# Performance work log

Hardware: AMD Instinct MI355X
Metric: run time of the kernel (lower is better)

The kernel has to match this reference:

```python
import jax, jax.numpy as jnp
import numpy as np

N, E, D, G = 50000, 600000, 128, 512  # nodes, edges, embed_dim, graphs-per-batch
LN_EPS = 1e-5


def setup_inputs() -> dict:
    key = jax.random.key(0)
    ks = jax.random.split(key, 8)
    node_hidden = jax.random.normal(ks[0], (N, D), dtype=jnp.float32)
    edge_hidden = jax.random.normal(ks[1], (E, D), dtype=jnp.float32)
    # GINEConv MLP params: Linear(D, 2D) -> ReLU -> Linear(2D, D)
    W1 = jax.random.normal(ks[2], (D, 2 * D), dtype=jnp.float32) * (1.0 / np.sqrt(D))
    b1 = jnp.zeros((2 * D,), dtype=jnp.float32)
    W2 = jax.random.normal(ks[3], (2 * D, D), dtype=jnp.float32) * (1.0 / np.sqrt(2 * D))
    b2 = jnp.zeros((D,), dtype=jnp.float32)
    ln_gamma = jnp.ones((D,), dtype=jnp.float32)
    ln_beta = jnp.zeros((D,), dtype=jnp.float32)
    edge_index = jax.random.randint(ks[4], (2, E), 0, N, dtype=jnp.int32)
    node_id = jnp.sort(jax.random.randint(ks[5], (N,), 0, G, dtype=jnp.int32))
    edge_id = jnp.sort(jax.random.randint(ks[6], (E,), 0, G, dtype=jnp.int32))
    return {
        "node_hidden": node_hidden, "edge_hidden": edge_hidden,
        "W1": W1, "b1": b1, "W2": W2, "b2": b2,
        "ln_gamma": ln_gamma, "ln_beta": ln_beta,
        "edge_index": edge_index, "node_id": node_id, "edge_id": edge_id,
    }


def reference(node_hidden, edge_hidden, W1, b1, W2, b2, ln_gamma, ln_beta,
              edge_index, node_id, edge_id):
    n = node_hidden.shape[0]
    src, dst = edge_index[0], edge_index[1]
    # --- GINEConv: msg = relu(x_src + e), scatter-add at dst, (1+eps)*x + agg, MLP ---
    msg = jax.nn.relu(node_hidden[src] + edge_hidden)          # [E, D]
    agg = jax.ops.segment_sum(msg, dst, num_segments=n)        # [N, D]
    h = node_hidden + agg                                      # eps = 0 (PyG default)
    h = jax.nn.relu(jnp.dot(h, W1) + b1)
    h = jnp.dot(h, W2) + b2                                    # [N, D]
    # --- LayerNorm over feature dim ---
    mu = jnp.mean(h, axis=-1, keepdims=True)
    var = jnp.mean(jnp.square(h - mu), axis=-1, keepdims=True)
    h = (h - mu) * jax.lax.rsqrt(var + LN_EPS) * ln_gamma + ln_beta
    # --- GraphNorm: divide each node's features by sqrt(#nodes in its graph) ---
    counts = jax.ops.segment_sum(jnp.ones((n,), dtype=h.dtype), node_id,
                                 num_segments=G)               # [G]
    scale = jax.lax.rsqrt(jnp.maximum(counts, 1.0))            # [G]
    h = h * scale[node_id][:, None]
    # --- last_act=True -> ReLU; dropout is identity in eval; residual add ---
    h = jax.nn.relu(h)
    return h + node_hidden
```

## Files before the change

### kernel.cpp

```cpp
#include <hip/hip_runtime.h>
#include <hip/hip_bf16.h>

#define N_NODES 50000
#define N_EDGES 600000
#define DIM     128
#define HID     256
#define NGRAPH  512
#define LN_EPS  1e-5f
#define CAP     48

typedef __attribute__((ext_vector_type(8))) short bf16x8;
typedef __attribute__((ext_vector_type(4))) float f32x4;

__device__ __forceinline__ unsigned short f2bf(float x) {
  unsigned int u = __builtin_bit_cast(unsigned int, x);
  unsigned int r = (u + 0x7FFFu + ((u >> 16) & 1u)) >> 16;
  return (unsigned short)r;
}

__device__ __forceinline__ float bf2f(unsigned int u) {
  return __builtin_bit_cast(float, u << 16);
}

__global__ void k_prep(const float* __restrict__ W1, const float* __restrict__ W2,
                       const float* __restrict__ nh,
                       unsigned char* __restrict__ blob,
                       unsigned short* __restrict__ nhb,
                       int* __restrict__ deg, int* __restrict__ counts) {
  int id = blockIdx.x * 256 + threadIdx.x;
  if (id < N_NODES) deg[id] = 0;
  if (id < NGRAPH) counts[id] = 0;
  if (id < (N_NODES * DIM) / 8) {
    const float4* s = (const float4*)nh + (size_t)id * 2;
    float4 a = s[0], b = s[1];
    union { unsigned short s8[8]; uint4 v; } u;
    u.s8[0] = f2bf(a.x); u.s8[1] = f2bf(a.y); u.s8[2] = f2bf(a.z); u.s8[3] = f2bf(a.w);
    u.s8[4] = f2bf(b.x); u.s8[5] = f2bf(b.y); u.s8[6] = f2bf(b.z); u.s8[7] = f2bf(b.w);
    *((uint4*)nhb + id) = u.v;
  }
  union { unsigned short s8[8]; uint4 v; } w;
  if (id < 4096) {
    int c  = id >> 4;
    int k0 = (id & 15) * 8;
#pragma unroll
    for (int j = 0; j < 8; ++j) w.s8[j] = f2bf(W1[(size_t)(k0 + j) * HID + c]);
    unsigned char* dst = blob + c * 256 + ((k0 * 2) ^ ((c & 7) << 4));
    *(uint4*)dst = w.v;
  } else if (id < 8192) {
    int id2 = id - 4096;
    int c  = id2 >> 5;
    int k0 = (id2 & 31) * 8;
#pragma unroll
    for (int j = 0; j < 8; ++j) w.s8[j] = f2bf(W2[(size_t)(k0 + j) * DIM + c]);
    unsigned char* dst = blob + 65536 + c * 512 + ((k0 * 2) ^ ((c & 7) << 4));
    *(uint4*)dst = w.v;
  }
}

__global__ void k_scatter(const int* __restrict__ ei, const int* __restrict__ node_id,
                          int* __restrict__ deg, int2* __restrict__ slots2,
                          int* __restrict__ counts) {
  int t = blockIdx.x * 256 + threadIdx.x;
  if (t < N_NODES) atomicAdd(&counts[node_id[t]], 1);
  if (t < N_EDGES) {
    int src = ei[t];
    int dst = ei[N_EDGES + t];
    int pos = atomicAdd(&deg[dst], 1);
    if (pos < CAP) slots2[(size_t)dst * CAP + pos] = make_int2(t, src);
  }
}

__global__ __launch_bounds__(512) void k_gather(
    const f32x4* __restrict__ nh4, const f32x4* __restrict__ eh4,
    const uint2* __restrict__ nhb2,
    const int* __restrict__ deg, const int2* __restrict__ slots2,
    uint2* __restrict__ hB2) {
  const int lane = threadIdx.x & 63;
  const int l31  = lane & 31;
  const int half = lane >> 5;
  const int nbase = (blockIdx.x * 8 + (threadIdx.x >> 6)) * 4;

  int dcur = 0;
  int2 scur = make_int2(0, 0);
  if (nbase < N_NODES) {
    dcur = deg[nbase];
    if (lane < CAP) scur = slots2[(size_t)nbase * CAP + lane];
  }
#pragma unroll
  for (int p = 0; p < 4; ++p) {
    int node = nbase + p;
    if (node >= N_NODES) break;
    int d = min(dcur, CAP);
    int2 s = scur;
    if (p < 3) {
      int nn = nbase + p + 1;
      if (nn < N_NODES) {
        dcur = deg[nn];
        if (lane < CAP) scur = slots2[(size_t)nn * CAP + lane];
      } else {
        dcur = 0;
      }
    }
    f32x4 acc = (f32x4){0.f, 0.f, 0.f, 0.f};
    if (half == 0) acc = nh4[(size_t)node * 32 + l31];
    int nloop = (d + 1) >> 1;
#pragma unroll 4
    for (int i = 0; i < nloop; ++i) {
      int idx = 2 * i + half;
      int ee = __shfl(s.x, idx);
      int ss = __shfl(s.y, idx);
      if (idx < d) {
        uint2 xb = nhb2[(size_t)ss * 32 + l31];
        f32x4 y = __builtin_nontemporal_load(&eh4[(size_t)ee * 32 + l31]);
        acc.x += fmaxf(bf2f(xb.x & 0xffffu) + y.x, 0.f);
        acc.y += fmaxf(bf2f(xb.x >> 16)     + y.y, 0.f);
        acc.z += fmaxf(bf2f(xb.y & 0xffffu) + y.z, 0.f);
        acc.w += fmaxf(bf2f(xb.y >> 16)     + y.w, 0.f);
      }
    }
    acc.x += __shfl_xor(acc.x, 32);
    acc.y += __shfl_xor(acc.y, 32);
    acc.z += __shfl_xor(acc.z, 32);
    acc.w += __shfl_xor(acc.w, 32);
    if (half == 0) {
      uint2 o;
      o.x = (unsigned)f2bf(acc.x) | ((unsigned)f2bf(acc.y) << 16);
      o.y = (unsigned)f2bf(acc.z) | ((unsigned)f2bf(acc.w) << 16);
      hB2[(size_t)node * 32 + l31] = o;
    }
  }
}

__global__ __launch_bounds__(512, 2) void k_mlp(
    const unsigned char* __restrict__ hB, const float* __restrict__ nh,
    const unsigned char* __restrict__ blob,
    const float* __restrict__ b1v, const float* __restrict__ b2v,
    const float* __restrict__ gam, const float* __restrict__ bet,
    const int* __restrict__ node_id, const int* __restrict__ counts,
    float* __restrict__ outp) {
  __shared__ unsigned char lds[131072];
  const int tid  = threadIdx.x;
  const int lane = tid & 63;
  const int wave = tid >> 6;
  const int l15  = lane & 15;
  const int lhi  = lane >> 4;
  const int swz  = (lane & 7) << 4;

  {
    const uint4* s = (const uint4*)blob;
    uint4* d = (uint4*)lds;
#pragma unroll
    for (int i = 0; i < 16; ++i) d[tid + i * 512] = s[tid + i * 512];
  }
  __syncthreads();

  const int row0 = blockIdx.x * 128 + wave * 16;
  const int arow = row0 + l15;
  const bool aok = arow < N_NODES;

  f32x4 c1[16];
#pragma unroll
  for (int i = 0; i < 16; ++i) c1[i] = (f32x4){0.f, 0.f, 0.f, 0.f};

#pragma unroll
  for (int ks = 0; ks < 4; ++ks) {
    bf16x8 af = (bf16x8){0, 0, 0, 0, 0, 0, 0, 0};
    if (aok) af = *(const bf16x8*)(hB + (size_t)arow * 256 + ks * 64 + lhi * 16);
#pragma unroll
    for (int ct = 0; ct < 16; ++ct) {
      int c = ct * 16 + l15;
      const bf16x8* bp = (const bf16x8*)(lds + c * 256 + ((ks * 64 + lhi * 16) ^ swz));
      c1[ct] = __builtin_amdgcn_mfma_f32_16x16x32_bf16(af, *bp, c1[ct], 0, 0, 0);
    }
  }
  __syncthreads();

  unsigned char* hb = lds + wave * 8192;
#pragma unroll
  for (int ct = 0; ct < 16; ++ct) {
    int c = ct * 16 + l15;
    float bb = b1v[c];
#pragma unroll
    for (int i = 0; i < 4; ++i) {
      int r = lhi * 4 + i;
      float v = fmaxf(c1[ct][i] + bb, 0.f);
      *(unsigned short*)(hb + r * 512 + ((2 * c) ^ ((r & 7) << 4))) = f2bf(v);
    }
  }
  __syncthreads();

  f32x4 c2[8];
#pragma unroll
  for (int i = 0; i < 8; ++i) c2[i] = (f32x4){0.f, 0.f, 0.f, 0.f};

#pragma unroll
  for (int ks = 0; ks < 8; ++ks) {
    bf16x8 af = *(const bf16x8*)(hb + l15 * 512 + ((ks * 64 + lhi * 16) ^ swz));
#pragma unroll
    for (int ct = 0; ct < 8; ++ct) {
      int c = ct * 16 + l15;
      const bf16x8* bp = (const bf16x8*)(lds + 65536 + c * 512 + ((ks * 64 + lhi * 16) ^ swz));
      c2[ct] = __builtin_amdgcn_mfma_f32_16x16x32_bf16(af, *bp, c2[ct], 0, 0, 0);
    }
  }

  float vbuf[8][4];
  float s[4] = {0.f, 0.f, 0.f, 0.f}, sq[4] = {0.f, 0.f, 0.f, 0.f};
#pragma unroll
  for (int ct = 0; ct < 8; ++ct) {
    float bb = b2v[ct * 16 + l15];
#pragma unroll
    for (int i = 0; i < 4; ++i) {
      float x = c2[ct][i] + bb;
      vbuf[ct][i] = x;
      s[i] += x;
      sq[i] += x * x;
    }
  }
#pragma unroll
  for (int m = 1; m <= 8; m <<= 1) {
#pragma unroll
    for (int i = 0; i < 4; ++i) {
      s[i] += __shfl_xor(s[i], m, 64);
      sq[i] += __shfl_xor(sq[i], m, 64);
    }
  }
  float mu[4], rstd[4], gs[4];
  int rr[4];
  bool rok[4];
#pragma unroll
  for (int i = 0; i < 4; ++i) {
    mu[i] = s[i] * (1.f / 128.f);
    float var = sq[i] * (1.f / 128.f) - mu[i] * mu[i];
    rstd[i] = rsqrtf(var + LN_EPS);
    rr[i] = row0 + lhi * 4 + i;
    rok[i] = rr[i] < N_NODES;
    int g = rok[i] ? node_id[rr[i]] : 0;
    gs[i] = rsqrtf(fmaxf((float)counts[g], 1.f));
  }
#pragma unroll
  for (int ct = 0; ct < 8; ++ct) {
    int c = ct * 16 + l15;
    float gg = gam[c], be = bet[c];
#pragma unroll
    for (int i = 0; i < 4; ++i) {
      if (rok[i]) {
        float y = (vbuf[ct][i] - mu[i]) * rstd[i] * gg + be;
        y *= gs[i];
        y = fmaxf(y, 0.f);
        y += nh[(size_t)rr[i] * DIM + c];
        outp[(size_t)rr[i] * DIM + c] = y;
      }
    }
  }
}

extern "C" void kernel_launch(void* const* d_in, const int* in_sizes, int n_in,
                              void* d_out, int out_size, void* d_ws, size_t ws_size,
                              hipStream_t stream) {
  const float* node_hidden = (const float*)d_in[0];
  const float* edge_hidden = (const float*)d_in[1];
  const float* W1  = (const float*)d_in[2];
  const float* b1  = (const float*)d_in[3];
  const float* W2  = (const float*)d_in[4];
  const float* b2  = (const float*)d_in[5];
  const float* lng = (const float*)d_in[6];
  const float* lnb = (const float*)d_in[7];
  const int* edge_index = (const int*)d_in[8];
  const int* node_id    = (const int*)d_in[9];
  float* out = (float*)d_out;

  unsigned char* ws = (unsigned char*)d_ws;
  unsigned char* blob = ws;
  int* counts   = (int*)(ws + 131072);
  int* deg      = (int*)(ws + 163840);
  int2* slots2  = (int2*)(ws + 393216);
  unsigned short* nhb = (unsigned short*)(ws + 33554432);
  unsigned char*  hB  = ws + 50331648;

  k_prep<<<3126, 256, 0, stream>>>(W1, W2, node_hidden, blob, nhb, deg, counts);
  k_scatter<<<2344, 256, 0, stream>>>(edge_index, node_id, deg, slots2, counts);
  k_gather<<<1563, 512, 0, stream>>>((const f32x4*)node_hidden,
                                     (const f32x4*)edge_hidden,
                                     (const uint2*)nhb,
                                     deg, slots2, (uint2*)hB);
  k_mlp<<<391, 512, 0, stream>>>(hB, node_hidden, blob, b1, b2, lng, lnb,
                                 node_id, counts, out);
}
```

Before: 190.0 us.

## Fuse prep and scatter kernels; gather four edges per wave with wider loads

The degree and count zeroing moves to a hipMemsetAsync, which lets the weight/node conversion kernel and the edge-scatter kernel merge into one launch. The gather kernel now splits each wave into four 16-lane groups, each handling one edge with 128-bit bf16 loads and two float4 edge loads, then reduces across the quarters with xor shuffles. Slot loads are limited to the valid degree, and the next node's degree is prefetched. The aim is fewer launches and more memory-level parallelism in the gather, at the cost of more registers and an extra memset.

```diff
diff --git a/kernel.cpp b/kernel.cpp
--- a/kernel.cpp
+++ b/kernel.cpp
@@ -22,14 +22,21 @@
   return __builtin_bit_cast(float, u << 16);
 }
 
-__global__ void k_prep(const float* __restrict__ W1, const float* __restrict__ W2,
-                       const float* __restrict__ nh,
-                       unsigned char* __restrict__ blob,
-                       unsigned short* __restrict__ nhb,
-                       int* __restrict__ deg, int* __restrict__ counts) {
+__global__ void k_prep_scatter(const float* __restrict__ W1, const float* __restrict__ W2,
+                               const float* __restrict__ nh,
+                               const int* __restrict__ ei, const int* __restrict__ node_id,
+                               unsigned char* __restrict__ blob,
+                               unsigned short* __restrict__ nhb,
+                               int* __restrict__ deg, int2* __restrict__ slots2,
+                               int* __restrict__ counts) {
   int id = blockIdx.x * 256 + threadIdx.x;
-  if (id < N_NODES) deg[id] = 0;
-  if (id < NGRAPH) counts[id] = 0;
+  if (id < N_NODES) atomicAdd(&counts[node_id[id]], 1);
+  if (id < N_EDGES) {
+    int src = ei[id];
+    int dst = ei[N_EDGES + id];
+    int pos = atomicAdd(&deg[dst], 1);
+    if (pos < CAP) slots2[(size_t)dst * CAP + pos] = make_int2(id, src);
+  }
   if (id < (N_NODES * DIM) / 8) {
     const float4* s = (const float4*)nh + (size_t)id * 2;
     float4 a = s[0], b = s[1];
@@ -57,76 +64,77 @@
   }
 }
 
-__global__ void k_scatter(const int* __restrict__ ei, const int* __restrict__ node_id,
-                          int* __restrict__ deg, int2* __restrict__ slots2,
-                          int* __restrict__ counts) {
-  int t = blockIdx.x * 256 + threadIdx.x;
-  if (t < N_NODES) atomicAdd(&counts[node_id[t]], 1);
-  if (t < N_EDGES) {
-    int src = ei[t];
-    int dst = ei[N_EDGES + t];
-    int pos = atomicAdd(&deg[dst], 1);
-    if (pos < CAP) slots2[(size_t)dst * CAP + pos] = make_int2(t, src);
-  }
-}
-
 __global__ __launch_bounds__(512) void k_gather(
     const f32x4* __restrict__ nh4, const f32x4* __restrict__ eh4,
-    const uint2* __restrict__ nhb2,
+    const uint4* __restrict__ nhb4,
     const int* __restrict__ deg, const int2* __restrict__ slots2,
-    uint2* __restrict__ hB2) {
-  const int lane = threadIdx.x & 63;
-  const int l31  = lane & 31;
-  const int half = lane >> 5;
-  const int nbase = (blockIdx.x * 8 + (threadIdx.x >> 6)) * 4;
-
-  int dcur = 0;
-  int2 scur = make_int2(0, 0);
-  if (nbase < N_NODES) {
-    dcur = deg[nbase];
-    if (lane < CAP) scur = slots2[(size_t)nbase * CAP + lane];
-  }
+    uint4* __restrict__ hB4) {
+  const int lane    = threadIdx.x & 63;
+  const int l15     = lane & 15;
+  const int quarter = lane >> 4;
+  const int nbase   = (blockIdx.x * 8 + (threadIdx.x >> 6)) * 4;
+  if (nbase >= N_NODES) return;
+
+  int d0 = deg[nbase];
+  int d1 = (nbase + 1 < N_NODES) ? deg[nbase + 1] : 0;
+  int2 s = make_int2(0, 0);
+  if (lane < min(d0, CAP)) s = slots2[(size_t)nbase * CAP + lane];
+
 #pragma unroll
   for (int p = 0; p < 4; ++p) {
     int node = nbase + p;
     if (node >= N_NODES) break;
-    int d = min(dcur, CAP);
-    int2 s = scur;
+    int d = min(d0, CAP);
+    int2 sc = s;
+    d0 = d1;
+    d1 = (node + 2 < N_NODES) ? deg[node + 2] : 0;
     if (p < 3) {
-      int nn = nbase + p + 1;
-      if (nn < N_NODES) {
-        dcur = deg[nn];
-        if (lane < CAP) scur = slots2[(size_t)nn * CAP + lane];
-      } else {
-        dcur = 0;
+      int nn = node + 1;
+      if (nn < N_NODES && lane < min(d0, CAP))
+        s = slots2[(size_t)nn * CAP + lane];
+      else
+        s = make_int2(0, 0);
+    }
+    f32x4 a0 = (f32x4){0.f, 0.f, 0.f, 0.f};
+    f32x4 a1 = (f32x4){0.f, 0.f, 0.f, 0.f};
+    if (quarter == 0) {
+      a0 = nh4[(size_t)node * 32 + 2 * l15];
+      a1 = nh4[(size_t)node * 32 + 2 * l15 + 1];
+    }
+    int nloop = (d + 3) >> 2;
+#pragma unroll 3
+    for (int i = 0; i < nloop; ++i) {
+      int idx = 4 * i + quarter;
+      int ee = __shfl(sc.x, idx);
+      int ss = __shfl(sc.y, idx);
+      if (idx < d) {
+        uint4 xb = nhb4[(size_t)ss * 16 + l15];
+        f32x4 y0 = __builtin_nontemporal_load(&eh4[(size_t)ee * 32 + 2 * l15]);
+        f32x4 y1 = __builtin_nontemporal_load(&eh4[(size_t)ee * 32 + 2 * l15 + 1]);
+        a0.x += fmaxf(bf2f(xb.x & 0xffffu) + y0.x, 0.f);
+        a0.y += fmaxf(bf2f(xb.x >> 16)     + y0.y, 0.f);
+        a0.z += fmaxf(bf2f(xb.y & 0xffffu) + y0.z, 0.f);
+        a0.w += fmaxf(bf2f(xb.y >> 16)     + y0.w, 0.f);
+        a1.x += fmaxf(bf2f(xb.z & 0xffffu) + y1.x, 0.f);
+        a1.y += fmaxf(bf2f(xb.z >> 16)     + y1.y, 0.f);
+        a1.z += fmaxf(bf2f(xb.w & 0xffffu) + y1.z, 0.f);
+        a1.w += fmaxf(bf2f(xb.w >> 16)     + y1.w, 0.f);
       }
     }
-    f32x4 acc = (f32x4){0.f, 0.f, 0.f, 0.f};
-    if (half == 0) acc = nh4[(size_t)node * 32 + l31];
-    int nloop = (d + 1) >> 1;
-#pragma unroll 4
-    for (int i = 0; i < nloop; ++i) {
-      int idx = 2 * i + half;
-      int ee = __shfl(s.x, idx);
-      int ss = __shfl(s.y, idx);
-      if (idx < d) {
-        uint2 xb = nhb2[(size_t)ss * 32 + l31];
-        f32x4 y = __builtin_nontemporal_load(&eh4[(size_t)ee * 32 + l31]);
-        acc.x += fmaxf(bf2f(xb.x & 0xffffu) + y.x, 0.f);
-        acc.y += fmaxf(bf2f(xb.x >> 16)     + y.y, 0.f);
-        acc.z += fmaxf(bf2f(xb.y & 0xffffu) + y.z, 0.f);
-        acc.w += fmaxf(bf2f(xb.y >> 16)     + y.w, 0.f);
-      }
-    }
-    acc.x += __shfl_xor(acc.x, 32);
-    acc.y += __shfl_xor(acc.y, 32);
-    acc.z += __shfl_xor(acc.z, 32);
-    acc.w += __shfl_xor(acc.w, 32);
-    if (half == 0) {
-      uint2 o;
-      o.x = (unsigned)f2bf(acc.x) | ((unsigned)f2bf(acc.y) << 16);
-      o.y = (unsigned)f2bf(acc.z) | ((unsigned)f2bf(acc.w) << 16);
-      hB2[(size_t)node * 32 + l31] = o;
+#pragma unroll
+    for (int m = 16; m <= 32; m <<= 1) {
+      a0.x += __shfl_xor(a0.x, m); a0.y += __shfl_xor(a0.y, m);
+      a0.z += __shfl_xor(a0.z, m); a0.w += __shfl_xor(a0.w, m);
+      a1.x += __shfl_xor(a1.x, m); a1.y += __shfl_xor(a1.y, m);
+      a1.z += __shfl_xor(a1.z, m); a1.w += __shfl_xor(a1.w, m);
+    }
+    if (quarter == 0) {
+      uint4 o;
+      o.x = (unsigned)f2bf(a0.x) | ((unsigned)f2bf(a0.y) << 16);
+      o.y = (unsigned)f2bf(a0.z) | ((unsigned)f2bf(a0.w) << 16);
+      o.z = (unsigned)f2bf(a1.x) | ((unsigned)f2bf(a1.y) << 16);
+      o.w = (unsigned)f2bf(a1.z) | ((unsigned)f2bf(a1.w) << 16);
+      hB4[(size_t)node * 16 + l15] = o;
     }
   }
 }
@@ -273,17 +281,19 @@
   unsigned char* ws = (unsigned char*)d_ws;
   unsigned char* blob = ws;
   int* counts   = (int*)(ws + 131072);
-  int* deg      = (int*)(ws + 163840);
+  int* deg      = (int*)(ws + 133120);
   int2* slots2  = (int2*)(ws + 393216);
   unsigned short* nhb = (unsigned short*)(ws + 33554432);
   unsigned char*  hB  = ws + 50331648;
 
-  k_prep<<<3126, 256, 0, stream>>>(W1, W2, node_hidden, blob, nhb, deg, counts);
-  k_scatter<<<2344, 256, 0, stream>>>(edge_index, node_id, deg, slots2, counts);
+  hipMemsetAsync(ws + 131072, 0, 2048 + 200000, stream);
+
+  k_prep_scatter<<<3126, 256, 0, stream>>>(W1, W2, node_hidden, edge_index, node_id,
+                                           blob, nhb, deg, slots2, counts);
   k_gather<<<1563, 512, 0, stream>>>((const f32x4*)node_hidden,
                                      (const f32x4*)edge_hidden,
-                                     (const uint2*)nhb,
-                                     deg, slots2, (uint2*)hB);
+                                     (const uint4*)nhb,
+                                     deg, slots2, (uint4*)hB);
   k_mlp<<<391, 512, 0, stream>>>(hB, node_hidden, blob, b1, b2, lng, lnb,
                                  node_id, counts, out);
 }
```

New measurement: 196.8 us. 3.6% more time.
